# Kernel optimization log

Hardware: AMD Instinct MI355X
Metric: run time of the kernel (lower is better)

The kernel has to match this reference:

```python
import jax, jax.numpy as jnp
import numpy as np

DIM, HEADS, DH = 512, 8, 64  # head_dim = DIM // HEADS, power of 2
BATCH, SEQ = 2, 1024
RANK = 4  # TensorTrain rank
EPS = 1e-8


def setup_inputs() -> dict:
    key = jax.random.key(0)
    ks = jax.random.split(key, 13)
    inp = {"x": jax.random.normal(ks[0], (BATCH, SEQ, DIM), jnp.float32)}
    i = 1
    for n in ("q", "k", "v", "o"):
        inp[n + "A"] = jax.random.normal(ks[i], (DIM, RANK), jnp.float32) * 0.1
        inp[n + "B"] = jax.random.normal(ks[i + 1], (RANK, DIM), jnp.float32) * 0.1
        inp[n + "b"] = jax.random.normal(ks[i + 2], (DIM,), jnp.float32) * 0.02
        i += 3
    return inp


def _tt_linear(x, A, Bm, b):
    # QuantumInspiredLinear: W = A @ Bm (rank-4 TT reconstruction), y = x W^T + b
    w = A @ Bm  # [out, in]
    return jnp.einsum('bsd,od->bso', x, w) + b


def _embed(x):
    # quantum state preparation: L2-normalize amplitudes per state
    return x / (jnp.linalg.norm(x, axis=-1, keepdims=True) + EPS)


def _measure(x):
    # measurement: squared amplitudes normalized to a probability distribution
    sq = x * x
    return sq / (jnp.sum(sq, axis=-1, keepdims=True) + EPS)


def reference(x, qA, qB, qb, kA, kB, kb, vA, vB, vb, oA, oB, ob):
    bsz, seq, dim = x.shape
    q = _tt_linear(x, qA, qB, qb).reshape(-1, DH)  # [N, dh], N = B*S*H
    k = _tt_linear(x, kA, kB, kb).reshape(-1, DH)
    v = _tt_linear(x, vA, vB, vb).reshape(-1, DH)
    qq = _embed(q)
    kq = _embed(k)
    # flat global attention over N = batch*seq*heads rows (as written in source)
    attn = jax.nn.softmax(jnp.matmul(qq, kq.T) / np.float32(np.sqrt(DH)), axis=-1)
    attended = jnp.matmul(attn, v)           # [N, dh]
    attended = _measure(attended)
    out = attended.reshape(bsz, seq, dim)    # [B, S, D]
    return _tt_linear(out, oA, oB, ob)
```

## Files before the change

### kernel.cpp

```cpp
#include <hip/hip_runtime.h>
#include <math.h>

#define DIM    512
#define RANK   4
#define NROW   2048
#define DH     64
#define NH     16384
#define EPS    1e-8f
#define EPSDEN2 2.68435456f
#define KSCALE 0.0626220703125f
#define C1 (2.0f * KSCALE)
#define C2 (2.0f * KSCALE * KSCALE)
#define KSPL 32

typedef short    bf16x8 __attribute__((ext_vector_type(8)));
typedef ushort   u16x8  __attribute__((ext_vector_type(8)));
typedef _Float16 half8  __attribute__((ext_vector_type(8)));
typedef float    f32x16 __attribute__((ext_vector_type(16)));

static __device__ __forceinline__ ushort f2bf(float f) {
    uint u = __float_as_uint(f);
    u += 0x7FFFu + ((u >> 16) & 1u);
    return (ushort)(u >> 16);
}
static __device__ __forceinline__ float bf2f(ushort u) {
    return __uint_as_float((uint)u << 16);
}
static __device__ __forceinline__ uint pkh2(float a, float b) {
    _Float16 ha = (_Float16)a, hb = (_Float16)b;
    return (uint)__builtin_bit_cast(ushort, ha) | ((uint)__builtin_bit_cast(ushort, hb) << 16);
}
static __device__ __forceinline__ float h2f(ushort u) {
    return (float)__builtin_bit_cast(_Float16, u);
}
static __device__ __forceinline__ void barrier_lgkm() {
    asm volatile("s_waitcnt lgkmcnt(0)" ::: "memory");
    __builtin_amdgcn_s_barrier();
}

__global__ __launch_bounds__(256) void proj_qkv(
    const float* __restrict__ x,
    const float* __restrict__ qA, const float* __restrict__ qB, const float* __restrict__ qb,
    const float* __restrict__ kA, const float* __restrict__ kB, const float* __restrict__ kb,
    const float* __restrict__ vA, const float* __restrict__ vB, const float* __restrict__ vb,
    ushort* __restrict__ qq_b, ushort* __restrict__ kqT, ushort* __restrict__ vvT)
{
    __shared__ float qrow[DIM], krow[DIM], vrowS[DIM];
    __shared__ float wred[4][12];
    __shared__ float tvals[12];
    __shared__ float norms[16];

    const int n = blockIdx.x, t = threadIdx.x;
    const int wid = t >> 6, lane = t & 63;

    const float x0 = x[n * DIM + t];
    const float x1 = x[n * DIM + t + 256];

    float p[12];
    #pragma unroll
    for (int r = 0; r < 4; ++r) {
        p[r]     = x0 * qB[r * DIM + t] + x1 * qB[r * DIM + t + 256];
        p[4 + r] = x0 * kB[r * DIM + t] + x1 * kB[r * DIM + t + 256];
        p[8 + r] = x0 * vB[r * DIM + t] + x1 * vB[r * DIM + t + 256];
    }
    #pragma unroll
    for (int i = 0; i < 12; ++i) {
        #pragma unroll
        for (int off = 32; off; off >>= 1) p[i] += __shfl_xor(p[i], off);
    }
    if (lane == 0) {
        #pragma unroll
        for (int i = 0; i < 12; ++i) wred[wid][i] = p[i];
    }
    __syncthreads();
    if (t < 12) tvals[t] = wred[0][t] + wred[1][t] + wred[2][t] + wred[3][t];
    __syncthreads();

    float tq[4], tk[4], tv[4];
    #pragma unroll
    for (int r = 0; r < 4; ++r) { tq[r] = tvals[r]; tk[r] = tvals[4 + r]; tv[r] = tvals[8 + r]; }

    #pragma unroll
    for (int h = 0; h < 2; ++h) {
        const int o = t + h * 256;
        float yq = qb[o], yk = kb[o], yv = vb[o];
        #pragma unroll
        for (int r = 0; r < 4; ++r) {
            yq += tq[r] * qA[o * RANK + r];
            yk += tk[r] * kA[o * RANK + r];
            yv += tv[r] * vA[o * RANK + r];
        }
        qrow[o] = yq; krow[o] = yk; vrowS[o] = yv;
    }
    __syncthreads();

    {
        const int c = t >> 5, i2 = t & 31;
        const float a  = qrow[c * 64 + i2], b2 = qrow[c * 64 + i2 + 32];
        const float ak = krow[c * 64 + i2], bk = krow[c * 64 + i2 + 32];
        float s  = a * a + b2 * b2;
        float sk = ak * ak + bk * bk;
        #pragma unroll
        for (int off = 16; off; off >>= 1) { s += __shfl_xor(s, off); sk += __shfl_xor(sk, off); }
        if (i2 == 0) { norms[c] = sqrtf(s); norms[8 + c] = sqrtf(sk); }
    }
    __syncthreads();

    #pragma unroll
    for (int h = 0; h < 2; ++h) {
        const int o = t + h * 256;
        const int c = o >> 6;
        qq_b[n * DIM + o] = f2bf(qrow[o] / (norms[c] + EPS));
    }

    if (t < 64) {
        uint pk[4], pv[4];
        #pragma unroll
        for (int i = 0; i < 4; ++i) {
            const float k0 = krow[(2 * i) * 64 + t]     / (norms[8 + 2 * i] + EPS);
            const float k1 = krow[(2 * i + 1) * 64 + t] / (norms[8 + 2 * i + 1] + EPS);
            pk[i] = pkh2(k0, k1);
            pv[i] = pkh2(vrowS[(2 * i) * 64 + t], vrowS[(2 * i + 1) * 64 + t]);
        }
        uint4 uk; uk.x = pk[0]; uk.y = pk[1]; uk.z = pk[2]; uk.w = pk[3];
        uint4 uv; uv.x = pv[0]; uv.y = pv[1]; uv.z = pv[2]; uv.w = pv[3];
        *(uint4*)((char*)kqT + (size_t)t * (NH * 2) + (size_t)n * 16) = uk;
        *(uint4*)((char*)vvT + (size_t)t * (NH * 2) + (size_t)n * 16) = uv;
    }
}

__global__ __launch_bounds__(256, 2) void phaseA(
    const ushort* __restrict__ kqT, const ushort* __restrict__ vvT,
    ushort* __restrict__ partA, ushort* __restrict__ partM1)
{
    __shared__ __align__(16) char smem[2][10240];
    constexpr int NSTA = 16;

    const int t = threadIdx.x;
    const int w = t >> 6, l = t & 63;
    const int l31 = l & 31, hi = l >> 5;
    const int agroup = blockIdx.x >> 5;
    const int ksplit = blockIdx.x & 31;
    const int kbase = ksplit * 512;
    const bool isM1 = (agroup == 16);
    const int a = isM1 ? 0 : (agroup * 4 + w);
    const bool compute = (!isM1) || (w == 0);

    const int srow = t >> 2, sslot = t & 3;
    const int woff = srow * 80 + sslot * 16;
    const size_t go = (size_t)srow * NH + kbase + sslot * 8;

    f32x16 acc[2][2];
    #pragma unroll
    for (int bt = 0; bt < 2; ++bt)
        #pragma unroll
        for (int dt = 0; dt < 2; ++dt)
            #pragma unroll
            for (int r = 0; r < 16; ++r) acc[bt][dt][r] = 0.f;

    uint4 kst = *(const uint4*)(kqT + go);
    uint4 vst = *(const uint4*)(vvT + go);
    *(uint4*)(smem[0] + woff) = kst;
    *(uint4*)(smem[0] + 5120 + woff) = vst;
    kst = *(const uint4*)(kqT + go + 32);
    vst = *(const uint4*)(vvT + go + 32);
    barrier_lgkm();

    for (int s = 0; s < NSTA; ++s) {
        const char* B = smem[s & 1];
        if (s + 1 < NSTA) {
            char* D = (char*)smem[(s & 1) ^ 1];
            *(uint4*)(D + woff) = kst;
            *(uint4*)(D + 5120 + woff) = vst;
        }
        if (s + 2 < NSTA) {
            kst = *(const uint4*)(kqT + go + (size_t)(s + 2) * 32);
            vst = *(const uint4*)(vvT + go + (size_t)(s + 2) * 32);
        }
        if (compute) {
            half8 af[2][2], vf[2][2];
            if (!isM1) {
                const half8 bc0 = *(const half8*)(B + a * 80 + hi * 16);
                const half8 bc1 = *(const half8*)(B + a * 80 + 32 + hi * 16);
                #pragma unroll
                for (int bt = 0; bt < 2; ++bt) {
                    af[bt][0] = (*(const half8*)(B + (bt * 32 + l31) * 80 + hi * 16)) * bc0;
                    af[bt][1] = (*(const half8*)(B + (bt * 32 + l31) * 80 + 32 + hi * 16)) * bc1;
                }
            } else {
                #pragma unroll
                for (int bt = 0; bt < 2; ++bt) {
                    af[bt][0] = *(const half8*)(B + (bt * 32 + l31) * 80 + hi * 16);
                    af[bt][1] = *(const half8*)(B + (bt * 32 + l31) * 80 + 32 + hi * 16);
                }
            }
            #pragma unroll
            for (int dt = 0; dt < 2; ++dt) {
                vf[dt][0] = *(const half8*)(B + 5120 + (dt * 32 + l31) * 80 + hi * 16);
                vf[dt][1] = *(const half8*)(B + 5120 + (dt * 32 + l31) * 80 + 32 + hi * 16);
            }
            #pragma unroll
            for (int bt = 0; bt < 2; ++bt)
                #pragma unroll
                for (int dt = 0; dt < 2; ++dt) {
                    acc[bt][dt] = __builtin_amdgcn_mfma_f32_32x32x16_f16(af[bt][0], vf[dt][0], acc[bt][dt], 0, 0, 0);
                    acc[bt][dt] = __builtin_amdgcn_mfma_f32_32x32x16_f16(af[bt][1], vf[dt][1], acc[bt][dt], 0, 0, 0);
                }
        }
        barrier_lgkm();
    }

    if (compute) {
        ushort* dst = isM1 ? (partM1 + (size_t)ksplit * 4096)
                           : (partA + ((size_t)(ksplit * 64 + a)) * 4096);
        #pragma unroll
        for (int bt = 0; bt < 2; ++bt)
            #pragma unroll
            for (int dt = 0; dt < 2; ++dt) {
                const int d = dt * 32 + l31;
                #pragma unroll
                for (int g = 0; g < 4; ++g) {
                    uint2 u2;
                    u2.x = pkh2(acc[bt][dt][4 * g],     acc[bt][dt][4 * g + 1]);
                    u2.y = pkh2(acc[bt][dt][4 * g + 2], acc[bt][dt][4 * g + 3]);
                    const int b0 = bt * 32 + 8 * g + 4 * hi;
                    *(uint2*)(dst + (size_t)d * 64 + b0) = u2;
                }
            }
    }
}

__global__ __launch_bounds__(256) void reduce_mom(
    const ushort* __restrict__ partA, const ushort* __restrict__ partM1,
    ushort* __restrict__ T2s, ushort* __restrict__ M1s, float* __restrict__ Vpart)
{
    const int blk = blockIdx.x, t = threadIdx.x;
    if (blk < 256) {
        const int g = blk * 256 + t;
        const uint2* src = (const uint2*)partA;
        float s0 = 0.f, s1 = 0.f, s2 = 0.f, s3 = 0.f;
        #pragma unroll
        for (int ks = 0; ks < KSPL; ++ks) {
            const uint2 u = src[(size_t)ks * 65536 + g];
            s0 += h2f((ushort)(u.x & 0xffff));
            s1 += h2f((ushort)(u.x >> 16));
            s2 += h2f((ushort)(u.y & 0xffff));
            s3 += h2f((ushort)(u.y >> 16));
        }
        uint2 o;
        o.x = (uint)f2bf(C2 * s0) | ((uint)f2bf(C2 * s1) << 16);
        o.y = (uint)f2bf(C2 * s2) | ((uint)f2bf(C2 * s3) << 16);
        ((uint2*)T2s)[g] = o;
        const int a  = g >> 10;
        const int d  = (g >> 4) & 63;
        const int b0 = (g & 15) * 4;
        if (a >= b0 && a < b0 + 4) {
            const int r = a - b0;
            const float sd = (r == 0) ? s0 : (r == 1) ? s1 : (r == 2) ? s2 : s3;
            Vpart[a * 64 + d] = sd;
        }
    } else {
        const int g = (blk - 256) * 256 + t;
        const uint2* src = (const uint2*)partM1;
        float s0 = 0.f, s1 = 0.f, s2 = 0.f, s3 = 0.f;
        #pragma unroll
        for (int ks = 0; ks < KSPL; ++ks) {
            const uint2 u = src[(size_t)ks * 1024 + g];
            s0 += h2f((ushort)(u.x & 0xffff));
            s1 += h2f((ushort)(u.x >> 16));
            s2 += h2f((ushort)(u.y & 0xffff));
            s3 += h2f((ushort)(u.y >> 16));
        }
        uint2 o;
        o.x = (uint)f2bf(C1 * s0) | ((uint)f2bf(C1 * s1) << 16);
        o.y = (uint)f2bf(C1 * s2) | ((uint)f2bf(C1 * s3) << 16);
        ((uint2*)M1s)[g] = o;
    }
}

__global__ __launch_bounds__(256, 3) void phaseB(
    const ushort* __restrict__ qq_b, const ushort* __restrict__ T2s,
    const ushort* __restrict__ M1s, float* __restrict__ numB)
{
    __shared__ float Lred[4][64][33];

    const int t = threadIdx.x;
    const int w = t >> 6, l = t & 63;
    const int l31 = l & 31, hi = l >> 5;
    const int q0 = blockIdx.x * 32;

    bf16x8 Qf[4];
    #pragma unroll
    for (int w16 = 0; w16 < 4; ++w16)
        Qf[w16] = *(const bf16x8*)((const char*)qq_b
            + (size_t)(q0 + l31) * 128 + w16 * 32 + hi * 16);

    float sv[16];
    {
        const uint4 u0 = *(const uint4*)(qq_b + (size_t)(q0 + l31) * 64 + w * 16);
        const uint4 u1 = *(const uint4*)(qq_b + (size_t)(q0 + l31) * 64 + w * 16 + 8);
        sv[0] = bf2f((ushort)(u0.x & 0xffff)); sv[1] = bf2f((ushort)(u0.x >> 16));
        sv[2] = bf2f((ushort)(u0.y & 0xffff)); sv[3] = bf2f((ushort)(u0.y >> 16));
        sv[4] = bf2f((ushort)(u0.z & 0xffff)); sv[5] = bf2f((ushort)(u0.z >> 16));
        sv[6] = bf2f((ushort)(u0.w & 0xffff)); sv[7] = bf2f((ushort)(u0.w >> 16));
        sv[8]  = bf2f((ushort)(u1.x & 0xffff)); sv[9]  = bf2f((ushort)(u1.x >> 16));
        sv[10] = bf2f((ushort)(u1.y & 0xffff)); sv[11] = bf2f((ushort)(u1.y >> 16));
        sv[12] = bf2f((ushort)(u1.z & 0xffff)); sv[13] = bf2f((ushort)(u1.z >> 16));
        sv[14] = bf2f((ushort)(u1.w & 0xffff)); sv[15] = bf2f((ushort)(u1.w >> 16));
    }

    f32x16 acc[2];
    #pragma unroll
    for (int dt = 0; dt < 2; ++dt)
        #pragma unroll
        for (int r = 0; r < 16; ++r) acc[dt][r] = 0.f;

    #pragma unroll 2
    for (int ai = 0; ai < 16; ++ai) {
        const char* base = (const char*)(T2s + (size_t)(w * 16 + ai) * 4096);
        #pragma unroll
        for (int dt = 0; dt < 2; ++dt) {
            bf16x8 af[4];
            #pragma unroll
            for (int w16 = 0; w16 < 4; ++w16)
                af[w16] = *(const bf16x8*)(base + (dt * 32 + l31) * 128 + w16 * 32 + hi * 16);
            f32x16 st;
            #pragma unroll
            for (int r = 0; r < 16; ++r) st[r] = 0.f;
            #pragma unroll
            for (int w16 = 0; w16 < 4; ++w16)
                st = __builtin_amdgcn_mfma_f32_32x32x16_bf16(af[w16], Qf[w16], st, 0, 0, 0);
            #pragma unroll
            for (int r = 0; r < 16; ++r)
                acc[dt][r] = fmaf(sv[ai], st[r], acc[dt][r]);
        }
    }

    if (w == 0) {
        #pragma unroll
        for (int dt = 0; dt < 2; ++dt) {
            bf16x8 af[4];
            #pragma unroll
            for (int w16 = 0; w16 < 4; ++w16)
                af[w16] = *(const bf16x8*)((const char*)M1s + (dt * 32 + l31) * 128 + w16 * 32 + hi * 16);
            f32x16 st;
            #pragma unroll
            for (int r = 0; r < 16; ++r) st[r] = 0.f;
            #pragma unroll
            for (int w16 = 0; w16 < 4; ++w16)
                st = __builtin_amdgcn_mfma_f32_32x32x16_bf16(af[w16], Qf[w16], st, 0, 0, 0);
            #pragma unroll
            for (int r = 0; r < 16; ++r) acc[dt][r] += st[r];
        }
    }

    #pragma unroll
    for (int dt = 0; dt < 2; ++dt)
        #pragma unroll
        for (int r = 0; r < 16; ++r) {
            const int d = dt * 32 + 8 * (r >> 2) + 4 * hi + (r & 3);
            Lred[w][d][l31] = acc[dt][r];
        }
    __syncthreads();

    {
        const int q = t >> 3, db = (t & 7) * 8;
        float s[8];
        #pragma unroll
        for (int i = 0; i < 8; ++i) {
            const int d = db + i;
            s[i] = (Lred[0][d][q] + Lred[1][d][q]) + (Lred[2][d][q] + Lred[3][d][q]);
        }
        float4 o0, o1;
        o0.x = s[0]; o0.y = s[1]; o0.z = s[2]; o0.w = s[3];
        o1.x = s[4]; o1.y = s[5]; o1.z = s[6]; o1.w = s[7];
        float* dst = numB + (size_t)(q0 + q) * 64 + db;
        *(float4*)dst = o0;
        *(float4*)(dst + 4) = o1;
    }
}

__global__ __launch_bounds__(256) void finalize(
    const float* __restrict__ numB, const float* __restrict__ Vpart,
    const float* __restrict__ oA, const float* __restrict__ oB,
    const float* __restrict__ ob, float* __restrict__ out)
{
    __shared__ float L[8][64];
    __shared__ float csum[8];
    __shared__ float wred[4][4];
    __shared__ float tvals[4];

    const int n = blockIdx.x, t = threadIdx.x;
    const int wid = t >> 6, lane = t & 63;

    {
        const int qs = t >> 5, d0 = (t & 31) * 2;
        const float2 f2 = *(const float2*)(numB + (size_t)(n * 8 + qs) * 64 + d0);
        L[qs][d0] = f2.x; L[qs][d0 + 1] = f2.y;
    }

    float vs = 0.f;
    #pragma unroll
    for (int a2 = 0; a2 < 64; ++a2) vs += Vpart[a2 * 64 + lane];
    __syncthreads();

    const float a0 = vs + L[wid][lane];
    const float a1 = vs + L[wid + 4][lane];

    float s0 = a0 * a0, s1 = a1 * a1;
    #pragma unroll
    for (int off = 32; off; off >>= 1) { s0 += __shfl_xor(s0, off); s1 += __shfl_xor(s1, off); }
    if (lane == 0) { csum[wid] = s0; csum[4 + wid] = s1; }
    __syncthreads();

    const float m0 = a0 * a0 / (csum[wid] + EPSDEN2);
    const float m1 = a1 * a1 / (csum[4 + wid] + EPSDEN2);

    float p[4];
    #pragma unroll
    for (int r = 0; r < 4; ++r) p[r] = m0 * oB[r * DIM + t] + m1 * oB[r * DIM + t + 256];
    #pragma unroll
    for (int r = 0; r < 4; ++r) {
        #pragma unroll
        for (int off = 32; off; off >>= 1) p[r] += __shfl_xor(p[r], off);
    }
    if (lane == 0) {
        #pragma unroll
        for (int r = 0; r < 4; ++r) wred[wid][r] = p[r];
    }
    __syncthreads();
    if (t < 4) tvals[t] = wred[0][t] + wred[1][t] + wred[2][t] + wred[3][t];
    __syncthreads();

    #pragma unroll
    for (int h = 0; h < 2; ++h) {
        const int o = t + h * 256;
        float y = ob[o];
        #pragma unroll
        for (int r = 0; r < 4; ++r) y += tvals[r] * oA[o * RANK + r];
        out[n * DIM + o] = y;
    }
}

extern "C" void kernel_launch(void* const* d_in, const int* in_sizes, int n_in,
                              void* d_out, int out_size, void* d_ws, size_t ws_size,
                              hipStream_t stream) {
    const float* x  = (const float*)d_in[0];
    const float* qA = (const float*)d_in[1];
    const float* qB = (const float*)d_in[2];
    const float* qb = (const float*)d_in[3];
    const float* kA = (const float*)d_in[4];
    const float* kB = (const float*)d_in[5];
    const float* kb = (const float*)d_in[6];
    const float* vA = (const float*)d_in[7];
    const float* vB = (const float*)d_in[8];
    const float* vb = (const float*)d_in[9];
    const float* oA = (const float*)d_in[10];
    const float* oB = (const float*)d_in[11];
    const float* ob = (const float*)d_in[12];

    ushort* qq_b   = (ushort*)d_ws;
    ushort* kqT    = qq_b + (size_t)NH * DH;
    ushort* vvT    = kqT + (size_t)NH * DH;
    ushort* T2s    = vvT + (size_t)NH * DH;
    ushort* M1s    = T2s + (size_t)64 * 4096;
    ushort* partM1 = M1s + 4096;
    float*  Vpart  = (float*)(partM1 + (size_t)KSPL * 4096);
    float*  numB   = (float*)(Vpart + 4096);
    ushort* partA  = (ushort*)numB;

    float* out = (float*)d_out;

    proj_qkv<<<NROW, 256, 0, stream>>>(x, qA, qB, qb, kA, kB, kb, vA, vB, vb, qq_b, kqT, vvT);
    phaseA<<<17 * KSPL, 256, 0, stream>>>(kqT, vvT, partA, partM1);
    reduce_mom<<<260, 256, 0, stream>>>(partA, partM1, T2s, M1s, Vpart);
    phaseB<<<512, 256, 0, stream>>>(qq_b, T2s, M1s, numB);
    finalize<<<NROW, 256, 0, stream>>>(numB, Vpart, oA, oB, ob, out);
}
```

Before: 86.56 us.

## Fuse finalize epilogue into phaseB to drop numB round trip and launch

Merges the finalize kernel (adding the V sum, measurement normalization, and the rank-4 output projection) into the phaseB epilogue. Each phaseB block already holds 32 head-rows, which is 4 full output rows, so it normalizes in registers and shared memory and writes the output directly. This removes the numB global write and read and one kernel launch. In exchange it adds shared memory and some serial work per phaseB block (the Vpart sum and the oB/oA loops), which may reduce occupancy.

Result: faster. 79.22 us (-8.5%).

```diff
diff --git a/kernel.cpp b/kernel.cpp
--- a/kernel.cpp
+++ b/kernel.cpp
@@ -280,14 +280,26 @@
 
 __global__ __launch_bounds__(256, 3) void phaseB(
     const ushort* __restrict__ qq_b, const ushort* __restrict__ T2s,
-    const ushort* __restrict__ M1s, float* __restrict__ numB)
+    const ushort* __restrict__ M1s, const float* __restrict__ Vpart,
+    const float* __restrict__ oA, const float* __restrict__ oB,
+    const float* __restrict__ ob, float* __restrict__ out)
 {
     __shared__ float Lred[4][64][33];
+    __shared__ float anum[32][65];
+    __shared__ float VsumL[64];
 
     const int t = threadIdx.x;
     const int w = t >> 6, l = t & 63;
     const int l31 = l & 31, hi = l >> 5;
     const int q0 = blockIdx.x * 32;
+    const int n0 = q0 >> 3;
+
+    if (w == 3) {
+        float vs = 0.f;
+        #pragma unroll
+        for (int a2 = 0; a2 < 64; ++a2) vs += Vpart[a2 * 64 + l];
+        VsumL[l] = vs;
+    }
 
     bf16x8 Qf[4];
     #pragma unroll
@@ -365,80 +377,50 @@
 
     {
         const int q = t >> 3, db = (t & 7) * 8;
-        float s[8];
+        float av[8];
+        float ss = 0.f;
         #pragma unroll
         for (int i = 0; i < 8; ++i) {
             const int d = db + i;
-            s[i] = (Lred[0][d][q] + Lred[1][d][q]) + (Lred[2][d][q] + Lred[3][d][q]);
-        }
-        float4 o0, o1;
-        o0.x = s[0]; o0.y = s[1]; o0.z = s[2]; o0.w = s[3];
-        o1.x = s[4]; o1.y = s[5]; o1.z = s[6]; o1.w = s[7];
-        float* dst = numB + (size_t)(q0 + q) * 64 + db;
-        *(float4*)dst = o0;
-        *(float4*)(dst + 4) = o1;
-    }
-}
-
-__global__ __launch_bounds__(256) void finalize(
-    const float* __restrict__ numB, const float* __restrict__ Vpart,
-    const float* __restrict__ oA, const float* __restrict__ oB,
-    const float* __restrict__ ob, float* __restrict__ out)
-{
-    __shared__ float L[8][64];
-    __shared__ float csum[8];
-    __shared__ float wred[4][4];
-    __shared__ float tvals[4];
-
-    const int n = blockIdx.x, t = threadIdx.x;
-    const int wid = t >> 6, lane = t & 63;
+            const float s = (Lred[0][d][q] + Lred[1][d][q])
+                          + (Lred[2][d][q] + Lred[3][d][q]) + VsumL[d];
+            av[i] = s;
+            ss = fmaf(s, s, ss);
+        }
+        ss += __shfl_xor(ss, 1);
+        ss += __shfl_xor(ss, 2);
+        ss += __shfl_xor(ss, 4);
+        const float inv = 1.f / (ss + EPSDEN2);
+        #pragma unroll
+        for (int i = 0; i < 8; ++i) anum[q][db + i] = av[i] * av[i] * inv;
+    }
+    __syncthreads();
 
     {
-        const int qs = t >> 5, d0 = (t & 31) * 2;
-        const float2 f2 = *(const float2*)(numB + (size_t)(n * 8 + qs) * 64 + d0);
-        L[qs][d0] = f2.x; L[qs][d0 + 1] = f2.y;
-    }
-
-    float vs = 0.f;
-    #pragma unroll
-    for (int a2 = 0; a2 < 64; ++a2) vs += Vpart[a2 * 64 + lane];
-    __syncthreads();
-
-    const float a0 = vs + L[wid][lane];
-    const float a1 = vs + L[wid + 4][lane];
-
-    float s0 = a0 * a0, s1 = a1 * a1;
-    #pragma unroll
-    for (int off = 32; off; off >>= 1) { s0 += __shfl_xor(s0, off); s1 += __shfl_xor(s1, off); }
-    if (lane == 0) { csum[wid] = s0; csum[4 + wid] = s1; }
-    __syncthreads();
-
-    const float m0 = a0 * a0 / (csum[wid] + EPSDEN2);
-    const float m1 = a1 * a1 / (csum[4 + wid] + EPSDEN2);
-
-    float p[4];
-    #pragma unroll
-    for (int r = 0; r < 4; ++r) p[r] = m0 * oB[r * DIM + t] + m1 * oB[r * DIM + t + 256];
-    #pragma unroll
-    for (int r = 0; r < 4; ++r) {
-        #pragma unroll
-        for (int off = 32; off; off >>= 1) p[r] += __shfl_xor(p[r], off);
-    }
-    if (lane == 0) {
-        #pragma unroll
-        for (int r = 0; r < 4; ++r) wred[wid][r] = p[r];
-    }
-    __syncthreads();
-    if (t < 4) tvals[t] = wred[0][t] + wred[1][t] + wred[2][t] + wred[3][t];
-    __syncthreads();
-
-    #pragma unroll
-    for (int h = 0; h < 2; ++h) {
-        const int o = t + h * 256;
-        float y = ob[o];
-        #pragma unroll
-        for (int r = 0; r < 4; ++r) y += tvals[r] * oA[o * RANK + r];
-        out[n * DIM + o] = y;
+        float p0 = 0.f, p1 = 0.f, p2 = 0.f, p3 = 0.f;
+        #pragma unroll
+        for (int h2 = 0; h2 < 8; ++h2) {
+            const int o = h2 * 64 + l;
+            const float m = anum[w * 8 + h2][l];
+            p0 = fmaf(m, oB[o],        p0);
+            p1 = fmaf(m, oB[512 + o],  p1);
+            p2 = fmaf(m, oB[1024 + o], p2);
+            p3 = fmaf(m, oB[1536 + o], p3);
+        }
+        #pragma unroll
+        for (int off = 32; off; off >>= 1) {
+            p0 += __shfl_xor(p0, off);
+            p1 += __shfl_xor(p1, off);
+            p2 += __shfl_xor(p2, off);
+            p3 += __shfl_xor(p3, off);
+        }
+        float* dstrow = out + (size_t)(n0 + w) * DIM;
+        #pragma unroll
+        for (int h2 = 0; h2 < 8; ++h2) {
+            const int o = h2 * 64 + l;
+            const float4 a4 = *(const float4*)(oA + o * RANK);
+            dstrow[o] = ob[o] + p0 * a4.x + p1 * a4.y + p2 * a4.z + p3 * a4.w;
+        }
     }
 }
 
@@ -466,14 +448,12 @@
     ushort* M1s    = T2s + (size_t)64 * 4096;
     ushort* partM1 = M1s + 4096;
     float*  Vpart  = (float*)(partM1 + (size_t)KSPL * 4096);
-    float*  numB   = (float*)(Vpart + 4096);
-    ushort* partA  = (ushort*)numB;
+    ushort* partA  = (ushort*)(Vpart + 4096);
 
     float* out = (float*)d_out;
 
     proj_qkv<<<NROW, 256, 0, stream>>>(x, qA, qB, qb, kA, kB, kb, vA, vB, vb, qq_b, kqT, vvT);
     phaseA<<<17 * KSPL, 256, 0, stream>>>(kqT, vvT, partA, partM1);
     reduce_mom<<<260, 256, 0, stream>>>(partA, partM1, T2s, M1s, Vpart);
-    phaseB<<<512, 256, 0, stream>>>(qq_b, T2s, M1s, numB);
-    finalize<<<NROW, 256, 0, stream>>>(numB, Vpart, oA, oB, ob, out);
-}
+    phaseB<<<512, 256, 0, stream>>>(qq_b, T2s, M1s, Vpart, oA, oB, ob, out);
+}
```
